# Optimization experiments

Measured on AMD Instinct MI355X. Metric: run time of the kernel, lower is better.

Reference implementation:

```python
import jax, jax.numpy as jnp
import numpy as np

EPS = 1e-5  # torch LayerNorm default
H, DH = 8, 64  # heads, dim_head


def _ln(x, g, b):
    mu = jnp.mean(x, axis=-1, keepdims=True)
    var = jnp.var(x, axis=-1, keepdims=True)
    return (x - mu) / jnp.sqrt(var + EPS) * g + b


def setup_inputs() -> dict:
    key = jax.random.key(0)
    ks = jax.random.split(key, 8)
    B, N, M, D, CD = 4, 2048, 256, 1024, 768
    J = M + 1 + N  # context + null + self
    return {
        "x": jax.random.normal(ks[0], (B, N, D), jnp.float32),
        "context": jax.random.normal(ks[1], (B, M, CD), jnp.float32),
        "att_bias": jax.random.normal(ks[2], (B, H, N, J), jnp.float32) * 0.02,
        "ln_g": jnp.ones((D,), jnp.float32),
        "ln_b": jnp.zeros((D,), jnp.float32),
        "null_kv": jax.random.normal(ks[3], (2, DH), jnp.float32),
        "Wq": jax.random.normal(ks[4], (D, H * DH), jnp.float32) * 0.02,
        "Wkv": jax.random.normal(ks[5], (D, 2 * DH), jnp.float32) * 0.02,
        "cln_g": jnp.ones((CD,), jnp.float32),
        "cln_b": jnp.zeros((CD,), jnp.float32),
        "Wc": jax.random.normal(ks[6], (CD, 2 * DH), jnp.float32) * 0.02,
        "bc": jnp.zeros((2 * DH,), jnp.float32),
        "Wo": jax.random.normal(ks[7], (H * DH, D), jnp.float32) * 0.02,
        "oln_g": jnp.ones((D,), jnp.float32),
        "oln_b": jnp.zeros((D,), jnp.float32),
    }


def reference(x, context, att_bias, ln_g, ln_b, null_kv, Wq, Wkv,
              cln_g, cln_b, Wc, bc, Wo, oln_g, oln_b):
    B, N, D = x.shape
    scale = DH ** -0.5
    xn = _ln(x, ln_g, ln_b)
    # queries: per-head [b,h,n,dh], pre-scaled
    q = (xn @ Wq).reshape(B, N, H, DH).transpose(0, 2, 1, 3) * scale
    # shared single-head k/v [b,n,dh]
    kv = xn @ Wkv
    k, v = kv[..., :DH], kv[..., DH:]
    # context k/v [b,m,dh]
    ckv = _ln(context, cln_g, cln_b) @ Wc + bc
    ck, cv = ckv[..., :DH], ckv[..., DH:]
    # null kv token [b,1,dh]
    nk = jnp.broadcast_to(null_kv[0], (B, 1, DH))
    nv = jnp.broadcast_to(null_kv[1], (B, 1, DH))
    # torch order: cat null first, then context -> (ck, nk, k)
    k = jnp.concatenate([ck, nk, k], axis=1)  # [b, j, dh]
    v = jnp.concatenate([cv, nv, v], axis=1)
    score = jnp.einsum('bhid,bjd->bhij', q, k) + att_bias
    probs = jax.nn.softmax(score.astype(jnp.float32), axis=-1).astype(v.dtype)
    att = jnp.einsum('bhij,bjd->bhid', probs, v)
    att = att.transpose(0, 2, 1, 3).reshape(B, N, H * DH)
    return _ln(att @ Wo, oln_g, oln_b)
```

## Files before the change

kernel.cpp:

```cpp
#include <hip/hip_runtime.h>
#include <hip/hip_bf16.h>
#include <cstdint>
#include <cstddef>

#define Bq  4
#define Nq  2048
#define Mq  256
#define Dq  1024
#define CDq 768
#define Hq  8
#define DHq 64
#define Jq  2305
#define QKVN 640
#define NCH 37
#define J2  (NCH * 64)

typedef __bf16  bf16x8 __attribute__((ext_vector_type(8)));
typedef float   f32x4  __attribute__((ext_vector_type(4)));
typedef float   f32x4u __attribute__((ext_vector_type(4), aligned(4)));
typedef float   f32x16 __attribute__((ext_vector_type(16)));
typedef short   s16x8  __attribute__((ext_vector_type(8)));
typedef short   s16x4  __attribute__((ext_vector_type(4)));
typedef unsigned int u32x4 __attribute__((ext_vector_type(4)));
typedef unsigned short u16;
typedef unsigned int   u32;

__device__ __forceinline__ u16 f2b(float v) {
  unsigned x = __builtin_bit_cast(unsigned, v);
  unsigned r = (x + 0x7fffu + ((x >> 16) & 1u)) >> 16;
  return (u16)r;
}
__device__ __forceinline__ float b2f(u16 u) {
  unsigned x = ((unsigned)u) << 16;
  return __builtin_bit_cast(float, x);
}
__device__ __forceinline__ u32 cvtpk(float lo, float hi) {
  u32 r;
  asm("v_cvt_pk_bf16_f32 %0, %1, %2" : "=v"(r) : "v"(lo), "v"(hi));
  return r;
}
__device__ __forceinline__ void pswap(u32& a, u32& b) {
  asm volatile("v_permlane32_swap_b32 %0, %1" : "+v"(a), "+v"(b));
}
__device__ __forceinline__ f32x4 mfma16(bf16x8 a, bf16x8 b, f32x4 c) {
  return __builtin_amdgcn_mfma_f32_16x16x32_bf16(a, b, c, 0, 0, 0);
}
__device__ __forceinline__ f32x16 mfma32(bf16x8 a, bf16x8 b, f32x16 c) {
  return __builtin_amdgcn_mfma_f32_32x32x16_bf16(a, b, c, 0, 0, 0);
}
__device__ __forceinline__ bf16x8 frag_ld(const u16* p) {
  return __builtin_bit_cast(bf16x8, *(const s16x8*)p);
}
__device__ __forceinline__ void stout(float* p, float v) { *p = v; }
__device__ __forceinline__ void stout(u16*   p, float v) { *p = f2b(v); }

__device__ __forceinline__ void gl_lds16(const void* gSrc, void* ldsDst) {
  __builtin_amdgcn_global_load_lds(
      (const __attribute__((address_space(1))) void*)gSrc,
      (__attribute__((address_space(3))) void*)ldsDst, 16, 0, 0);
}

__global__ __launch_bounds__(256) void prep_kernel(
    const float* __restrict__ x,   const float* __restrict__ ln_g,
    const float* __restrict__ ln_b, u16* __restrict__ xn,
    const float* __restrict__ ctx, const float* __restrict__ cln_g,
    const float* __restrict__ cln_b, u16* __restrict__ ctxn,
    const float* __restrict__ Wq, const float* __restrict__ Wkv,
    const float* __restrict__ Wc, const float* __restrict__ Wo,
    u16* __restrict__ WqkvT, u16* __restrict__ WcT, u16* __restrict__ WoT) {
  const int tid = threadIdx.x;
  if (blockIdx.x < Bq * Nq + Bq * Mq) {
    const int row = blockIdx.x;
    const float* in; const float* g; const float* bb; u16* out; int D;
    if (row < Bq * Nq) {
      in = x + (size_t)row * Dq; g = ln_g; bb = ln_b;
      out = xn + (size_t)row * Dq; D = Dq;
    } else {
      int r2 = row - Bq * Nq;
      in = ctx + (size_t)r2 * CDq; g = cln_g; bb = cln_b;
      out = ctxn + (size_t)r2 * CDq; D = CDq;
    }
    __shared__ float buf[1024];
    __shared__ float red[8];
    float s = 0.f, s2 = 0.f;
    for (int i = tid; i < D; i += 256) {
      float v = in[i];
      buf[i] = v;
      s += v; s2 += v * v;
    }
    #pragma unroll
    for (int off = 32; off; off >>= 1) {
      s  += __shfl_down(s,  off);
      s2 += __shfl_down(s2, off);
    }
    if ((tid & 63) == 0) { red[tid >> 6] = s; red[4 + (tid >> 6)] = s2; }
    __syncthreads();
    float sum = red[0] + red[1] + red[2] + red[3];
    float sq  = red[4] + red[5] + red[6] + red[7];
    float mean = sum / D;
    float var  = sq / D - mean * mean;
    float rstd = rsqrtf(var + 1e-5f);
    for (int i = tid; i < D; i += 256)
      out[i] = f2b((buf[i] - mean) * rstd * g[i] + bb[i]);
  } else {
    __shared__ float T[32][33];
    int bid = blockIdx.x - (Bq * Nq + Bq * Mq);
    const float* W; u16* WT; int K, N, bx, by;
    if (bid < 512)      { W = Wq;  WT = WqkvT;                    K = 1024; N = 512;  bx = bid % 16;        by = bid / 16; }
    else if (bid < 640) { W = Wkv; WT = WqkvT + (size_t)512*1024; K = 1024; N = 128;  bx = (bid-512) % 4;   by = (bid-512) / 4; }
    else if (bid < 736) { W = Wc;  WT = WcT;                      K = 768;  N = 128;  bx = (bid-640) % 4;   by = (bid-640) / 4; }
    else                { W = Wo;  WT = WoT;                      K = 512;  N = 1024; bx = (bid-736) % 32;  by = (bid-736) / 32; }
    const int n0 = bx * 32, k0 = by * 32;
    const int tx = tid & 31, ty = tid >> 5;
    #pragma unroll
    for (int i = 0; i < 32; i += 8)
      T[ty + i][tx] = W[(size_t)(k0 + ty + i) * N + n0 + tx];
    __syncthreads();
    #pragma unroll
    for (int i = 0; i < 32; i += 8)
      WT[(size_t)(n0 + ty + i) * K + k0 + tx] = f2b(T[tx][ty + i]);
  }
}

__global__ __launch_bounds__(256) void ln_out_kernel(
    const u16* __restrict__ in, const float* __restrict__ g,
    const float* __restrict__ bb, float* __restrict__ out) {
  const int row = blockIdx.x;
  const int tid = threadIdx.x;
  __shared__ float buf[1024];
  __shared__ float red[8];
  const u16* xr = in + (size_t)row * Dq;
  float s = 0.f, s2 = 0.f;
  {
    s16x4 v4 = *(const s16x4*)(xr + tid * 4);
    #pragma unroll
    for (int e = 0; e < 4; ++e) {
      float v = b2f((u16)v4[e]);
      buf[tid * 4 + e] = v;
      s += v; s2 += v * v;
    }
  }
  #pragma unroll
  for (int off = 32; off; off >>= 1) {
    s  += __shfl_down(s,  off);
    s2 += __shfl_down(s2, off);
  }
  if ((tid & 63) == 0) { red[tid >> 6] = s; red[4 + (tid >> 6)] = s2; }
  __syncthreads();
  float sum = red[0] + red[1] + red[2] + red[3];
  float sq  = red[4] + red[5] + red[6] + red[7];
  float mean = sum / Dq;
  float var  = sq / Dq - mean * mean;
  float rstd = rsqrtf(var + 1e-5f);
  #pragma unroll
  for (int e = 0; e < 4; ++e) {
    int i = tid * 4 + e;
    out[(size_t)row * Dq + i] = (buf[i] - mean) * rstd * g[i] + bb[i];
  }
}

template <typename OT>
__device__ __forceinline__ void gemm_body(const u16* __restrict__ A,
                                          const u16* __restrict__ BT,
                                          OT* __restrict__ C,
                                          int N, int K, int m0, int n0,
                                          u16* Al, u16* Bl) {
  const int tid  = threadIdx.x;
  const int lane = tid & 63, wave = tid >> 6;
  const int l16  = lane & 15, lhi = lane >> 4;
  const int wm = (wave >> 1) * 64, wn = (wave & 1) * 64;

  const int offB = (wave << 10) + (lane << 4);
  const int srow = offB >> 6;
  const int scby = offB & 63;

  f32x4 acc[4][4];
  #pragma unroll
  for (int i = 0; i < 4; ++i)
    #pragma unroll
    for (int j = 0; j < 4; ++j) acc[i][j] = f32x4{0.f, 0.f, 0.f, 0.f};

  for (int k0 = 0; k0 < K; k0 += 32) {
    __syncthreads();
    #pragma unroll
    for (int c = 0; c < 2; ++c) {
      gl_lds16((const char*)(A  + (size_t)(m0 + srow + c * 64) * K + k0) + scby,
               (char*)Al + c * 4096 + (wave << 10));
      gl_lds16((const char*)(BT + (size_t)(n0 + srow + c * 64) * K + k0) + scby,
               (char*)Bl + c * 4096 + (wave << 10));
    }
    __syncthreads();

    bf16x8 af[4], bfr[4];
    #pragma unroll
    for (int mt = 0; mt < 4; ++mt)
      af[mt] = frag_ld(Al + (wm + mt * 16 + l16) * 32 + lhi * 8);
    #pragma unroll
    for (int nt = 0; nt < 4; ++nt)
      bfr[nt] = frag_ld(Bl + (wn + nt * 16 + l16) * 32 + lhi * 8);
    __builtin_amdgcn_s_setprio(1);
    #pragma unroll
    for (int mt = 0; mt < 4; ++mt)
      #pragma unroll
      for (int nt = 0; nt < 4; ++nt)
        acc[mt][nt] = mfma16(af[mt], bfr[nt], acc[mt][nt]);
    __builtin_amdgcn_s_setprio(0);
  }

  #pragma unroll
  for (int mt = 0; mt < 4; ++mt)
    #pragma unroll
    for (int nt = 0; nt < 4; ++nt)
      #pragma unroll
      for (int r = 0; r < 4; ++r)
        stout(C + (size_t)(m0 + wm + mt * 16 + lhi * 4 + r) * N
                + (n0 + wn + nt * 16 + l16),
              acc[mt][nt][r]);
}

__global__ __launch_bounds__(256) void gemm_qkv_ckv(
    const u16* __restrict__ xn, const u16* __restrict__ WqkvT,
    u16* __restrict__ qkv,
    const u16* __restrict__ ctxn, const u16* __restrict__ WcT,
    u16* __restrict__ ckvb) {
  const u16 *A, *BT; u16* C; int N, K, m0, n0;
  if (blockIdx.y < 5) {
    A = xn; BT = WqkvT; C = qkv; N = QKVN; K = Dq;
    m0 = blockIdx.x * 128; n0 = blockIdx.y * 128;
  } else {
    if (blockIdx.x >= 8) return;
    A = ctxn; BT = WcT; C = ckvb; N = 2 * DHq; K = CDq;
    m0 = blockIdx.x * 128; n0 = 0;
  }
  __shared__ __align__(16) u16 Al[128 * 32];
  __shared__ __align__(16) u16 Bl[128 * 32];
  gemm_body<u16>(A, BT, C, N, K, m0, n0, Al, Bl);
}

__global__ __launch_bounds__(256) void gemm128b(const u16* __restrict__ A,
                                                const u16* __restrict__ BT,
                                                u16* __restrict__ C,
                                                int N, int K) {
  __shared__ __align__(16) u16 Al[128 * 32];
  __shared__ __align__(16) u16 Bl[128 * 32];
  gemm_body<u16>(A, BT, C, N, K, blockIdx.x * 128, blockIdx.y * 128, Al, Bl);
}

__global__ void build_kv(const u16* __restrict__ qkv,
                         const u16* __restrict__ ckvb,
                         const float* __restrict__ nullkv,
                         const float* __restrict__ bc,
                         u16* __restrict__ Kt, u16* __restrict__ Vt) {
  int idx = blockIdx.x * 256 + threadIdx.x;
  if (idx >= Bq * J2 * 64) return;
  int d = idx & 63;
  int t = idx >> 6;
  int j = t % J2;
  int b = t / J2;
  float k = 0.f, v = 0.f;
  if (j < Mq) {
    const u16* p = ckvb + (size_t)(b * Mq + j) * 128;
    k = b2f(p[d])      + bc[d];
    v = b2f(p[64 + d]) + bc[64 + d];
  } else if (j == Mq) {
    k = nullkv[d];
    v = nullkv[64 + d];
  } else if (j < Jq) {
    const u16* p = qkv + (size_t)(b * Nq + (j - Mq - 1)) * QKVN + 512;
    k = b2f(p[d]);
    v = b2f(p[64 + d]);
  }
  int ch = j >> 6, row = j & 63;
  char* tbase = (char*)Kt + ((size_t)(b * NCH + ch)) * 8192;
  *(u16*)(tbase + row * 128 + ((d << 1) ^ ((row & 7) << 4))) = f2b(k);
  char* vbase = (char*)Vt + ((size_t)(b * NCH + ch)) * 8192;
  *(u16*)(vbase + d * 128 + ((row << 1) ^ ((d & 7) << 4))) = f2b(v);
}

__global__ __launch_bounds__(512) void attn_kernel(
    const u16* __restrict__ qkv, const u16* __restrict__ Kt,
    const u16* __restrict__ Vt, const float* __restrict__ bias,
    u16* __restrict__ att) {
  __shared__ __align__(16) u16 Kl [2][4096];
  __shared__ __align__(16) u16 VTl[2][4096];
  const int tid  = threadIdx.x;
  const int wave = tid >> 6, lane = tid & 63;
  const int l = lane & 31, hi = lane >> 5;
  const int qt = blockIdx.x, b = blockIdx.z;
  const int h = wave;
  const int qrow0 = qt * 32;

  bf16x8 qf[4];
  {
    const u16* qp = qkv + ((size_t)(b * Nq + qrow0 + l)) * QKVN
                        + h * DHq + hi * 8;
    #pragma unroll
    for (int kt = 0; kt < 4; ++kt) qf[kt] = frag_ld(qp + kt * 16);
  }

  float m_s = -INFINITY, l_s = 0.f;
  f32x16 oacc[2];
  #pragma unroll
  for (int dt = 0; dt < 2; ++dt)
    #pragma unroll
    for (int r = 0; r < 16; ++r) oacc[dt][r] = 0.f;

  const float* bp = bias
      + ((size_t)((b * Hq + h) * (size_t)Nq + qrow0 + l)) * Jq + 4 * hi;

  const size_t tb0 = (size_t)b * NCH;
  const int soff = (wave << 10) + (lane << 4);

  auto stage = [&](int buf, int ch) {
    const char* kt_ = (const char*)Kt + (tb0 + ch) * 8192 + soff;
    const char* vt_ = (const char*)Vt + (tb0 + ch) * 8192 + soff;
    gl_lds16(kt_, (char*)&Kl[buf][0]  + (wave << 10));
    gl_lds16(vt_, (char*)&VTl[buf][0] + (wave << 10));
  };

  auto loadBias = [&](f32x4 (&bv)[2][4], int ch) {
    const int jc = ch * 64;
    if (ch < NCH - 1) {
      #pragma unroll
      for (int jt = 0; jt < 2; ++jt)
        #pragma unroll
        for (int g = 0; g < 4; ++g)
          bv[jt][g] = (f32x4)(*(const f32x4u*)(bp + jc + jt * 32 + 8 * g));
    } else {
      #pragma unroll
      for (int jt = 0; jt < 2; ++jt)
        #pragma unroll
        for (int g = 0; g < 4; ++g)
          #pragma unroll
          for (int e = 0; e < 4; ++e) {
            int jg = jc + jt * 32 + 8 * g + 4 * hi + e;
            bv[jt][g][e] = (jg < Jq) ? bp[jc + jt * 32 + 8 * g + e] : -1e30f;
          }
    }
  };

  f32x4 bvA[2][4], bvB[2][4];
  stage(0, 0);
  loadBias(bvA, 0);
  __syncthreads();

  auto body = [&](int ch, f32x4 (&bvC)[2][4], f32x4 (&bvN)[2][4]) {
    const int cur = ch & 1;
    if (ch + 1 < NCH) {
      stage(cur ^ 1, ch + 1);
      loadBias(bvN, ch + 1);
    }
    const char* kbase = (const char*)&Kl[cur][0];
    const char* vbase = (const char*)&VTl[cur][0];

    f32x16 sacc[2];
    #pragma unroll
    for (int jt = 0; jt < 2; ++jt)
      #pragma unroll
      for (int r = 0; r < 16; ++r) sacc[jt][r] = 0.f;
    __builtin_amdgcn_s_setprio(1);
    #pragma unroll
    for (int jt = 0; jt < 2; ++jt) {
      const int row = jt * 32 + l;
      const int sw = (row & 7) << 4;
      #pragma unroll
      for (int kt = 0; kt < 4; ++kt) {
        bf16x8 kf = frag_ld((const u16*)(kbase + row * 128
                                         + ((kt * 32 + hi * 16) ^ sw)));
        sacc[jt] = mfma32(kf, qf[kt], sacc[jt]);
      }
    }
    __builtin_amdgcn_s_setprio(0);

    #pragma unroll
    for (int jt = 0; jt < 2; ++jt)
      #pragma unroll
      for (int r = 0; r < 16; ++r)
        sacc[jt][r] = sacc[jt][r] * 0.125f + bvC[jt][r >> 2][r & 3];

    float pmax = sacc[0][0];
    #pragma unroll
    for (int jt = 0; jt < 2; ++jt)
      #pragma unroll
      for (int r = 0; r < 16; ++r) pmax = fmaxf(pmax, sacc[jt][r]);
    pmax = fmaxf(pmax, __shfl_xor(pmax, 32));

    if (__any(pmax > m_s + 8.f)) {
      float mnew = fmaxf(m_s, pmax);
      float corr = __expf(m_s - mnew);
      l_s *= corr;
      m_s = mnew;
      #pragma unroll
      for (int r = 0; r < 16; ++r) {
        float c = __shfl(corr, (r & 3) + 8 * (r >> 2) + 4 * hi);
        oacc[0][r] *= c;
        oacc[1][r] *= c;
      }
    }

    float ps = 0.f;
    #pragma unroll
    for (int jt = 0; jt < 2; ++jt)
      #pragma unroll
      for (int r = 0; r < 16; ++r) {
        float pv = __expf(sacc[jt][r] - m_s);
        sacc[jt][r] = pv;
        ps += pv;
      }
    ps += __shfl_xor(ps, 32);
    l_s += ps;

    u32 pk[2][8];
    #pragma unroll
    for (int jt = 0; jt < 2; ++jt)
      #pragma unroll
      for (int g = 0; g < 4; ++g) {
        pk[jt][2 * g]     = cvtpk(sacc[jt][4 * g],     sacc[jt][4 * g + 1]);
        pk[jt][2 * g + 1] = cvtpk(sacc[jt][4 * g + 2], sacc[jt][4 * g + 3]);
      }

    #pragma unroll
    for (int kt = 0; kt < 4; ++kt) {
      const int t = kt & 1, js = kt >> 1;
      u32 a0 = pk[js][4 * t],     b0 = pk[js][4 * t + 2];
      u32 a1 = pk[js][4 * t + 1], b1 = pk[js][4 * t + 3];
      pswap(a0, b0);
      pswap(a1, b1);
      bf16x8 paf = __builtin_bit_cast(bf16x8, u32x4{a0, a1, b0, b1});
      __builtin_amdgcn_s_setprio(1);
      #pragma unroll
      for (int dt = 0; dt < 2; ++dt) {
        const int vrow = dt * 32 + l;
        bf16x8 vf = frag_ld((const u16*)(vbase + vrow * 128
                     + ((kt * 32 + hi * 16) ^ ((vrow & 7) << 4))));
        oacc[dt] = mfma32(paf, vf, oacc[dt]);
      }
      __builtin_amdgcn_s_setprio(0);
    }
    __syncthreads();
  };

  int ch = 0;
  while (true) {
    body(ch, bvA, bvB);
    if (++ch == NCH) break;
    body(ch, bvB, bvA);
    if (++ch == NCH) break;
  }

  float linv = 1.0f / l_s;
  #pragma unroll
  for (int r = 0; r < 16; ++r) {
    const int qo = (r & 3) + 8 * (r >> 2) + 4 * hi;
    float inv = __shfl(linv, qo);
    u16* op = att + ((size_t)(b * Nq + qrow0 + qo)) * (Hq * DHq) + h * DHq + l;
    op[0]  = f2b(oacc[0][r] * inv);
    op[32] = f2b(oacc[1][r] * inv);
  }
}

extern "C" void kernel_launch(void* const* d_in, const int* in_sizes, int n_in,
                              void* d_out, int out_size, void* d_ws, size_t ws_size,
                              hipStream_t stream) {
  const float* x       = (const float*)d_in[0];
  const float* context = (const float*)d_in[1];
  const float* att_bias= (const float*)d_in[2];
  const float* ln_g    = (const float*)d_in[3];
  const float* ln_b    = (const float*)d_in[4];
  const float* null_kv = (const float*)d_in[5];
  const float* Wq      = (const float*)d_in[6];
  const float* Wkv     = (const float*)d_in[7];
  const float* cln_g   = (const float*)d_in[8];
  const float* cln_b   = (const float*)d_in[9];
  const float* Wc      = (const float*)d_in[10];
  const float* bc      = (const float*)d_in[11];
  const float* Wo      = (const float*)d_in[12];
  const float* oln_g   = (const float*)d_in[13];
  const float* oln_b   = (const float*)d_in[14];
  float* out = (float*)d_out;

  char* p = (char*)d_ws;
  auto alloc = [&](size_t bytes) {
    void* r = (void*)p;
    p += (bytes + 255) & ~(size_t)255;
    return r;
  };
  u16* xn     = (u16*)alloc((size_t)Bq * Nq * Dq * 2);
  u16* ctxn   = (u16*)alloc((size_t)Bq * Mq * CDq * 2);
  u16* WqkvT  = (u16*)alloc((size_t)QKVN * Dq * 2);
  u16* WcT    = (u16*)alloc((size_t)2 * DHq * CDq * 2);
  u16* WoT    = (u16*)alloc((size_t)Dq * Hq * DHq * 2);
  u16* qkv    = (u16*)alloc((size_t)Bq * Nq * QKVN * 2);
  u16* ckvb   = (u16*)alloc((size_t)Bq * Mq * 2 * DHq * 2);
  u16* Ktil   = (u16*)alloc((size_t)Bq * NCH * 8192);
  u16* Vtil   = (u16*)alloc((size_t)Bq * NCH * 8192);
  u16* attb   = (u16*)alloc((size_t)Bq * Nq * Hq * DHq * 2);
  u16* y      = (u16*)alloc((size_t)Bq * Nq * Dq * 2);

  prep_kernel<<<Bq * Nq + Bq * Mq + 1248, 256, 0, stream>>>(
      x, ln_g, ln_b, xn, context, cln_g, cln_b, ctxn,
      Wq, Wkv, Wc, Wo, WqkvT, WcT, WoT);

  gemm_qkv_ckv<<<dim3(Bq * Nq / 128, 6), 256, 0, stream>>>(
      xn, WqkvT, qkv, ctxn, WcT, ckvb);

  build_kv<<<(Bq * J2 * 64 + 255) / 256, 256, 0, stream>>>(
      qkv, ckvb, null_kv, bc, Ktil, Vtil);

  attn_kernel<<<dim3(Nq / 32, 1, Bq), 512, 0, stream>>>(
      qkv, Ktil, Vtil, att_bias, attb);

  gemm128b<<<dim3(Bq * Nq / 128, Dq / 128), 256, 0, stream>>>(
      attb, WoT, y, Dq, Hq * DHq);
  ln_out_kernel<<<Bq * Nq, 256, 0, stream>>>(y, oln_g, oln_b, out);
}
```

Baseline: 249.6 us.

## Fuse output projection and output LayerNorm into attention kernel epilogue

The attention kernel now writes its normalized per-head outputs into a shared-memory tile and multiplies that 32x512 tile by the transposed Wo directly with MFMA. Each wave produces 128 output columns, and the output LayerNorm is applied through a cross-wave reduction in shared memory. This drops the separate GEMM and LN launches along with the bf16 round trips of the attention output and the projected activations. In exchange, each block reads all of WoT from global or L2 memory without LDS staging, and shared-memory and register use go up, which may lower occupancy.

Result: no change. 249.4 us (-0.0%).

```diff
diff --git a/kernel.cpp b/kernel.cpp
--- a/kernel.cpp
+++ b/kernel.cpp
@@ -122,43 +122,6 @@
   }
 }
 
-__global__ __launch_bounds__(256) void ln_out_kernel(
-    const u16* __restrict__ in, const float* __restrict__ g,
-    const float* __restrict__ bb, float* __restrict__ out) {
-  const int row = blockIdx.x;
-  const int tid = threadIdx.x;
-  __shared__ float buf[1024];
-  __shared__ float red[8];
-  const u16* xr = in + (size_t)row * Dq;
-  float s = 0.f, s2 = 0.f;
-  {
-    s16x4 v4 = *(const s16x4*)(xr + tid * 4);
-    #pragma unroll
-    for (int e = 0; e < 4; ++e) {
-      float v = b2f((u16)v4[e]);
-      buf[tid * 4 + e] = v;
-      s += v; s2 += v * v;
-    }
-  }
-  #pragma unroll
-  for (int off = 32; off; off >>= 1) {
-    s  += __shfl_down(s,  off);
-    s2 += __shfl_down(s2, off);
-  }
-  if ((tid & 63) == 0) { red[tid >> 6] = s; red[4 + (tid >> 6)] = s2; }
-  __syncthreads();
-  float sum = red[0] + red[1] + red[2] + red[3];
-  float sq  = red[4] + red[5] + red[6] + red[7];
-  float mean = sum / Dq;
-  float var  = sq / Dq - mean * mean;
-  float rstd = rsqrtf(var + 1e-5f);
-  #pragma unroll
-  for (int e = 0; e < 4; ++e) {
-    int i = tid * 4 + e;
-    out[(size_t)row * Dq + i] = (buf[i] - mean) * rstd * g[i] + bb[i];
-  }
-}
-
 template <typename OT>
 __device__ __forceinline__ void gemm_body(const u16* __restrict__ A,
                                           const u16* __restrict__ BT,
@@ -235,15 +198,6 @@
   __shared__ __align__(16) u16 Al[128 * 32];
   __shared__ __align__(16) u16 Bl[128 * 32];
   gemm_body<u16>(A, BT, C, N, K, m0, n0, Al, Bl);
-}
-
-__global__ __launch_bounds__(256) void gemm128b(const u16* __restrict__ A,
-                                                const u16* __restrict__ BT,
-                                                u16* __restrict__ C,
-                                                int N, int K) {
-  __shared__ __align__(16) u16 Al[128 * 32];
-  __shared__ __align__(16) u16 Bl[128 * 32];
-  gemm_body<u16>(A, BT, C, N, K, blockIdx.x * 128, blockIdx.y * 128, Al, Bl);
 }
 
 __global__ void build_kv(const u16* __restrict__ qkv,
@@ -280,12 +234,17 @@
 __global__ __launch_bounds__(512) void attn_kernel(
     const u16* __restrict__ qkv, const u16* __restrict__ Kt,
     const u16* __restrict__ Vt, const float* __restrict__ bias,
-    u16* __restrict__ att) {
+    const u16* __restrict__ WoT, const float* __restrict__ oln_g,
+    const float* __restrict__ oln_b, float* __restrict__ out) {
   __shared__ __align__(16) u16 Kl [2][4096];
   __shared__ __align__(16) u16 VTl[2][4096];
+  __shared__ __align__(16) u16 attT[32][520];
+  __shared__ float redS[8][32];
+  __shared__ float redQ[8][32];
   const int tid  = threadIdx.x;
   const int wave = tid >> 6, lane = tid & 63;
   const int l = lane & 31, hi = lane >> 5;
+  const int l16 = lane & 15, lhi = lane >> 4;
   const int qt = blockIdx.x, b = blockIdx.z;
   const int h = wave;
   const int qrow0 = qt * 32;
@@ -448,14 +407,94 @@
     if (++ch == NCH) break;
   }
 
-  float linv = 1.0f / l_s;
-  #pragma unroll
-  for (int r = 0; r < 16; ++r) {
-    const int qo = (r & 3) + 8 * (r >> 2) + 4 * hi;
-    float inv = __shfl(linv, qo);
-    u16* op = att + ((size_t)(b * Nq + qrow0 + qo)) * (Hq * DHq) + h * DHq + l;
-    op[0]  = f2b(oacc[0][r] * inv);
-    op[32] = f2b(oacc[1][r] * inv);
+  {
+    float linv = 1.0f / l_s;
+    #pragma unroll
+    for (int r = 0; r < 16; ++r) {
+      const int qo = (r & 3) + 8 * (r >> 2) + 4 * hi;
+      float inv = __shfl(linv, qo);
+      attT[qo][h * 64 + l]      = f2b(oacc[0][r] * inv);
+      attT[qo][h * 64 + 32 + l] = f2b(oacc[1][r] * inv);
+    }
+  }
+  __syncthreads();
+
+  const int n0w = wave * 128;
+  f32x4 acc2[2][8];
+  #pragma unroll
+  for (int mt = 0; mt < 2; ++mt)
+    #pragma unroll
+    for (int nt = 0; nt < 8; ++nt) acc2[mt][nt] = f32x4{0.f, 0.f, 0.f, 0.f};
+
+  for (int k0 = 0; k0 < 16; ++k0) {
+    bf16x8 af[2];
+    #pragma unroll
+    for (int mt = 0; mt < 2; ++mt)
+      af[mt] = frag_ld(&attT[mt * 16 + l16][k0 * 32 + lhi * 8]);
+    __builtin_amdgcn_s_setprio(1);
+    #pragma unroll
+    for (int nt = 0; nt < 8; ++nt) {
+      bf16x8 bfr = frag_ld(WoT + (size_t)(n0w + nt * 16 + l16) * 512
+                               + k0 * 32 + lhi * 8);
+      acc2[0][nt] = mfma16(af[0], bfr, acc2[0][nt]);
+      acc2[1][nt] = mfma16(af[1], bfr, acc2[1][nt]);
+    }
+    __builtin_amdgcn_s_setprio(0);
+  }
+
+  float psum[8], psq[8];
+  #pragma unroll
+  for (int i = 0; i < 8; ++i) { psum[i] = 0.f; psq[i] = 0.f; }
+  #pragma unroll
+  for (int mt = 0; mt < 2; ++mt)
+    #pragma unroll
+    for (int nt = 0; nt < 8; ++nt)
+      #pragma unroll
+      for (int r = 0; r < 4; ++r) {
+        float v = acc2[mt][nt][r];
+        psum[mt * 4 + r] += v;
+        psq[mt * 4 + r]  += v * v;
+      }
+  #pragma unroll
+  for (int off = 1; off < 16; off <<= 1)
+    #pragma unroll
+    for (int i = 0; i < 8; ++i) {
+      psum[i] += __shfl_xor(psum[i], off);
+      psq[i]  += __shfl_xor(psq[i],  off);
+    }
+  if (l16 == 0) {
+    #pragma unroll
+    for (int mt = 0; mt < 2; ++mt)
+      #pragma unroll
+      for (int r = 0; r < 4; ++r) {
+        redS[wave][mt * 16 + lhi * 4 + r] = psum[mt * 4 + r];
+        redQ[wave][mt * 16 + lhi * 4 + r] = psq[mt * 4 + r];
+      }
+  }
+  __syncthreads();
+
+  float gv[8], bbv[8];
+  #pragma unroll
+  for (int nt = 0; nt < 8; ++nt) {
+    gv[nt]  = oln_g[n0w + nt * 16 + l16];
+    bbv[nt] = oln_b[n0w + nt * 16 + l16];
+  }
+  #pragma unroll
+  for (int mt = 0; mt < 2; ++mt) {
+    #pragma unroll
+    for (int r = 0; r < 4; ++r) {
+      const int row = mt * 16 + lhi * 4 + r;
+      float s = 0.f, q2 = 0.f;
+      #pragma unroll
+      for (int w = 0; w < 8; ++w) { s += redS[w][row]; q2 += redQ[w][row]; }
+      float mean = s * (1.0f / Dq);
+      float var  = q2 * (1.0f / Dq) - mean * mean;
+      float rstd = rsqrtf(var + 1e-5f);
+      float* op = out + ((size_t)(b * Nq + qrow0 + row)) * Dq + n0w;
+      #pragma unroll
+      for (int nt = 0; nt < 8; ++nt)
+        op[nt * 16 + l16] = (acc2[mt][nt][r] - mean) * rstd * gv[nt] + bbv[nt];
+    }
   }
 }
 
@@ -494,8 +533,6 @@
   u16* ckvb   = (u16*)alloc((size_t)Bq * Mq * 2 * DHq * 2);
   u16* Ktil   = (u16*)alloc((size_t)Bq * NCH * 8192);
   u16* Vtil   = (u16*)alloc((size_t)Bq * NCH * 8192);
-  u16* attb   = (u16*)alloc((size_t)Bq * Nq * Hq * DHq * 2);
-  u16* y      = (u16*)alloc((size_t)Bq * Nq * Dq * 2);
 
   prep_kernel<<<Bq * Nq + Bq * Mq + 1248, 256, 0, stream>>>(
       x, ln_g, ln_b, xn, context, cln_g, cln_b, ctxn,
@@ -508,9 +545,5 @@
       qkv, ckvb, null_kv, bc, Ktil, Vtil);
 
   attn_kernel<<<dim3(Nq / 32, 1, Bq), 512, 0, stream>>>(
-      qkv, Ktil, Vtil, att_bias, attb);
-
-  gemm128b<<<dim3(Bq * Nq / 128, Dq / 128), 256, 0, stream>>>(
-      attb, WoT, y, Dq, Hq * DHq);
-  ln_out_kernel<<<Bq * Nq, 256, 0, stream>>>(y, oln_g, oln_b, out);
-}
+      qkv, Ktil, Vtil, att_bias, WoT, oln_g, oln_b, out);
+}
```
